# Optimization experiments

Measured on AMD Instinct MI355X. Metric: run time of the kernel, lower is better.

## Reference

```python
import jax, jax.numpy as jnp
import numpy as np

B, S, DIM, H, C = 1, 1024, 4096, 32, 8
HD = DIM // H  # 128
NEG = -1e9


def setup_inputs() -> dict:
    key = jax.random.key(0)
    ks = jax.random.split(key, 8)
    scale = 0.02
    x = jax.random.normal(ks[0], (B, S, DIM), jnp.float32)
    wq = jax.random.normal(ks[1], (DIM, DIM), jnp.float32) * scale
    wk = jax.random.normal(ks[2], (DIM, DIM), jnp.float32) * scale
    wv = jax.random.normal(ks[3], (DIM, DIM), jnp.float32) * scale
    wo = jax.random.normal(ks[4], (DIM, DIM), jnp.float32) * scale
    # RoPE tables (theta=10000), matching precompute_freqs_cis
    inv = 1.0 / (10000.0 ** (np.arange(0, HD, 2, dtype=np.float32) / HD))  # [HD/2]
    ang = np.arange(S, dtype=np.float32)[:, None] * inv[None, :]  # [S, HD/2]
    freqs_cos = jnp.asarray(np.cos(ang))
    freqs_sin = jnp.asarray(np.sin(ang))
    # causal mask used at prefill (start_pos == 0)
    mask = jnp.where(jnp.triu(jnp.ones((S, S), bool), k=1), jnp.float32(NEG), 0.0)
    # cluster labels: ensure every cluster non-empty; rep = first head with label
    rng = np.random.default_rng(0)
    lab = np.concatenate([np.arange(C), rng.integers(0, C, H - C)]).astype(np.int32)
    rep = np.array([np.where(lab == c)[0][0] for c in range(C)], dtype=np.int32)
    return {
        "x": x, "wq": wq, "wk": wk, "wv": wv, "wo": wo,
        "freqs_cos": freqs_cos, "freqs_sin": freqs_sin, "mask": mask,
        "cluster_assignment": jnp.asarray(lab), "rep_heads": jnp.asarray(rep),
        "start_pos": 0,
    }


def _rope(x, cos, sin):
    # x: [b, s, h, d]; cos/sin: [s, d/2]; interleaved complex multiply
    xr, xi = x[..., ::2], x[..., 1::2]
    cos = cos[None, :, None, :]
    sin = sin[None, :, None, :]
    orr = xr * cos - xi * sin
    oi = xr * sin + xi * cos
    return jnp.stack([orr, oi], axis=-1).reshape(x.shape)


def reference(x, wq, wk, wv, wo, freqs_cos, freqs_sin, mask,
              cluster_assignment, rep_heads, start_pos):
    b, s, dim = x.shape
    h, d = H, HD
    xq = (x @ wq.T).reshape(b, s, h, d)
    xk = (x @ wk.T).reshape(b, s, h, d)
    xv = (x @ wv.T).reshape(b, s, h, d)
    xq = _rope(xq, freqs_cos, freqs_sin)
    xk = _rope(xk, freqs_cos, freqs_sin)
    xqh = jnp.transpose(xq, (0, 2, 1, 3))  # [b, h, s, d]
    xkh = jnp.transpose(xk, (0, 2, 1, 3))
    vh = jnp.transpose(xv, (0, 2, 1, 3))
    # CHAI: gather representative head per cluster, score once per cluster
    xq_new = xqh[:, rep_heads]  # [b, C, s, d]
    xk_new = xkh[:, rep_heads]
    sc = jnp.einsum("bcqd,bckd->bcqk", xq_new, xk_new) / jnp.sqrt(jnp.float32(d))
    # scatter cluster scores back to every member head (pure gather by label)
    scores = sc[:, cluster_assignment]  # [b, h, s, s]
    scores = scores + mask[None, None]
    p = jax.nn.softmax(scores.astype(jnp.float32), axis=-1).astype(x.dtype)
    out = jnp.einsum("bhqk,bhkd->bhqd", p, vh)
    out = jnp.transpose(out, (0, 2, 1, 3)).reshape(b, s, h * d)
    return out @ wo.T
```

## Files before the change

kernel.cpp:

```cpp
#include <hip/hip_runtime.h>

typedef __bf16 bf16x8 __attribute__((ext_vector_type(8)));
typedef float f32x4 __attribute__((ext_vector_type(4)));

#define BM 128
#define BN 128
#define BK 64

__device__ __forceinline__ unsigned short f2bf(float f) {
    union { float f; unsigned int u; } x; x.f = f;
    unsigned int u = x.u;
    u += 0x7fffu + ((u >> 16) & 1u);
    return (unsigned short)(u >> 16);
}

__device__ __forceinline__ float bf2f(unsigned short h) {
    union { unsigned int u; float f; } x; x.u = ((unsigned int)h) << 16;
    return x.f;
}

__device__ __forceinline__ void async_copy16(const void* g, void* l) {
    __builtin_amdgcn_global_load_lds(
        (const __attribute__((address_space(1))) void*)(uintptr_t)g,
        (__attribute__((address_space(3))) void*)(uintptr_t)l, 16, 0, 0);
}

__global__ void cvt_all(const float* __restrict__ x, const float* __restrict__ wq,
                        const float* __restrict__ wk, const float* __restrict__ wv,
                        const float* __restrict__ wo, const int* __restrict__ rep,
                        unsigned short* __restrict__ xb, unsigned short* __restrict__ wqkvb,
                        unsigned short* __restrict__ wob) {
    long i = (long)blockIdx.x * 256 + threadIdx.x;
    const float* src;
    unsigned short* dst;
    long j;
    if (i < 1048576) {
        j = i;
        src = x; dst = xb;
    } else if (i < 7340032) {
        j = i - 1048576;
        int r = (int)(j >> 10), c4 = (int)(j & 1023);
        const float* s;
        if (r < 1024)      s = wq + ((long)(rep[r >> 7] * 128 + (r & 127)) << 12);
        else if (r < 2048) s = wk + ((long)(rep[(r - 1024) >> 7] * 128 + (r & 127)) << 12);
        else               s = wv + ((long)(r - 2048) << 12);
        float4 v = ((const float4*)s)[c4];
        ushort4 o = { f2bf(v.x), f2bf(v.y), f2bf(v.z), f2bf(v.w) };
        ((ushort4*)(wqkvb + ((long)r << 12)))[c4] = o;
        return;
    } else {
        j = i - 7340032;
        src = wo; dst = wob;
    }
    float4 v = ((const float4*)src)[j];
    ushort4 o = { f2bf(v.x), f2bf(v.y), f2bf(v.z), f2bf(v.w) };
    ((ushort4*)dst)[j] = o;
}


template<bool F32OUT, int MODE>
__global__ __launch_bounds__(256, 2) void gemm_bt(
    const unsigned short* __restrict__ A, const unsigned short* __restrict__ B,
    void* __restrict__ Cv, int K, int lda, int ldb, int ldc,
    long long aZ, long long bZ, long long cZ, const int* __restrict__ aIdx,
    int kOffZ, int nby) {
    __shared__ unsigned short As[BM * BK];
    __shared__ unsigned short Bs[BN * BK];

    int L = blockIdx.x;
    int q8 = gridDim.x >> 3;
    int wk_ = (L & 7) * q8 + (L >> 3);
    int bmi = wk_ & 7;
    int t2 = wk_ >> 3;
    int bni = t2 % nby;
    int z = t2 / nby;

    if (MODE == 1 && bni > bmi) return;

    A += (aIdx ? (long long)aIdx[z] : (long long)z) * aZ;
    B += (long long)z * bZ;
    int bm = bmi * BM;
    int bn = bni * BN;
    int t = threadIdx.x;
    int lane = t & 63;
    int w = t >> 6;
    int wr = (w >> 1) * 64, wc = (w & 1) * 64;

    int kt0 = z * kOffZ;
    int kEnd = kt0 + K;
    if (MODE == 2) kEnd = kt0 + min(K, bm + BM);

    f32x4 acc[4][4] = {};

    for (int kt = kt0; kt < kEnd; kt += BK) {
#pragma unroll
        for (int i = 0; i < 4; ++i) {
            int f = i * 256 + t;
            int row = f >> 3;
            int c8 = f & 7;
            async_copy16(A + (long)(bm + row) * lda + kt + c8 * 8, &As[f * 8]);
            async_copy16(B + (long)(bn + row) * ldb + kt + c8 * 8, &Bs[f * 8]);
        }
        asm volatile("s_waitcnt vmcnt(0)" ::: "memory");
        __syncthreads();
#pragma unroll
        for (int kk = 0; kk < BK; kk += 32) {
            bf16x8 a[4], b[4];
            int r0 = lane & 15;
            int kof = kk + ((lane >> 4) << 3);
#pragma unroll
            for (int m = 0; m < 4; ++m)
                a[m] = *(const bf16x8*)&As[(wr + m * 16 + r0) * BK + kof];
#pragma unroll
            for (int n = 0; n < 4; ++n)
                b[n] = *(const bf16x8*)&Bs[(wc + n * 16 + r0) * BK + kof];
#pragma unroll
            for (int m = 0; m < 4; ++m)
#pragma unroll
                for (int n = 0; n < 4; ++n)
                    acc[m][n] = __builtin_amdgcn_mfma_f32_16x16x32_bf16(a[m], b[n], acc[m][n], 0, 0, 0);
        }
        __syncthreads();
    }

    int cl = lane & 15;
    int rbase = (lane >> 4) << 2;
    if (F32OUT) {
        float* C = (float*)Cv + (long long)z * cZ;
#pragma unroll
        for (int m = 0; m < 4; ++m)
#pragma unroll
            for (int n = 0; n < 4; ++n)
#pragma unroll
                for (int j = 0; j < 4; ++j)
                    C[(long)(bm + wr + m * 16 + rbase + j) * ldc + (bn + wc + n * 16 + cl)] = acc[m][n][j];
    } else {
        unsigned short* C = (unsigned short*)Cv + (long long)z * cZ;
#pragma unroll
        for (int m = 0; m < 4; ++m)
#pragma unroll
            for (int n = 0; n < 4; ++n)
#pragma unroll
                for (int j = 0; j < 4; ++j)
                    C[(long)(bm + wr + m * 16 + rbase + j) * ldc + (bn + wc + n * 16 + cl)] = f2bf(acc[m][n][j]);
    }
}

__global__ void reduce_rope(unsigned short* __restrict__ qkv,
                            const float* __restrict__ fc, const float* __restrict__ fs,
                            int nsplit) {
    int s = blockIdx.y;
    int cc = (blockIdx.x * 256 + threadIdx.x) * 8;
    long base = (long)s * 6144 + cc;
    ushort4 a0 = *(const ushort4*)(qkv + base);
    ushort4 a1 = *(const ushort4*)(qkv + base + 4);
    float f[8] = { bf2f(a0.x), bf2f(a0.y), bf2f(a0.z), bf2f(a0.w),
                   bf2f(a1.x), bf2f(a1.y), bf2f(a1.z), bf2f(a1.w) };
    for (int z = 1; z < nsplit; ++z) {
        const unsigned short* p = qkv + (long)z * 6291456;
        ushort4 b0 = *(const ushort4*)(p + base);
        ushort4 b1 = *(const ushort4*)(p + base + 4);
        f[0] += bf2f(b0.x); f[1] += bf2f(b0.y); f[2] += bf2f(b0.z); f[3] += bf2f(b0.w);
        f[4] += bf2f(b1.x); f[5] += bf2f(b1.y); f[6] += bf2f(b1.z); f[7] += bf2f(b1.w);
    }
    if (cc < 2048) {
        int i0 = (cc & 127) >> 1;
        const float* cp = fc + (s << 6) + i0;
        const float* sp = fs + (s << 6) + i0;
#pragma unroll
        for (int p = 0; p < 4; ++p) {
            float co = cp[p], sn = sp[p];
            float x0 = f[2 * p], x1 = f[2 * p + 1];
            f[2 * p] = x0 * co - x1 * sn;
            f[2 * p + 1] = x0 * sn + x1 * co;
        }
    }
    ushort4 o0 = { f2bf(f[0]), f2bf(f[1]), f2bf(f[2]), f2bf(f[3]) };
    ushort4 o1 = { f2bf(f[4]), f2bf(f[5]), f2bf(f[6]), f2bf(f[7]) };
    *(ushort4*)(qkv + base) = o0;
    *(ushort4*)(qkv + base + 4) = o1;
}

__global__ void reduce_out4(const unsigned short* __restrict__ p, float* __restrict__ out) {
    long i = (long)blockIdx.x * 256 + threadIdx.x;
    ushort4 a = ((const ushort4*)p)[i];
    ushort4 b = ((const ushort4*)(p + 4194304))[i];
    ushort4 c = ((const ushort4*)(p + 8388608))[i];
    ushort4 d = ((const ushort4*)(p + 12582912))[i];
    float4 o;
    o.x = bf2f(a.x) + bf2f(b.x) + bf2f(c.x) + bf2f(d.x);
    o.y = bf2f(a.y) + bf2f(b.y) + bf2f(c.y) + bf2f(d.y);
    o.z = bf2f(a.z) + bf2f(b.z) + bf2f(c.z) + bf2f(d.z);
    o.w = bf2f(a.w) + bf2f(b.w) + bf2f(c.w) + bf2f(d.w);
    ((float4*)out)[i] = o;
}

__global__ void transpose_v(const unsigned short* __restrict__ qkv, unsigned short* __restrict__ vt) {
    __shared__ unsigned short tile[32][33];
    int h = blockIdx.z, d0 = blockIdx.x * 32, s0 = blockIdx.y * 32;
    int tx = threadIdx.x & 31, ty = threadIdx.x >> 5;
#pragma unroll
    for (int i = 0; i < 32; i += 8)
        tile[ty + i][tx] = qkv[(long)(s0 + ty + i) * 6144 + 2048 + h * 128 + d0 + tx];
    __syncthreads();
#pragma unroll
    for (int i = 0; i < 32; i += 8)
        vt[(long)h * 131072 + (long)(d0 + ty + i) * 1024 + s0 + tx] = tile[tx][ty + i];
}

__global__ __launch_bounds__(256) void softmax_causal(const float* __restrict__ sc,
                                                      unsigned short* __restrict__ P) {
    int i = blockIdx.x;
    int c = blockIdx.y;
    long base = ((long)c << 20) + ((long)i << 10);
    const float* row = sc + base;
    unsigned short* prow = P + base;
    int t = threadIdx.x;
    const float alpha = 0.08838834764831845f;
    int nj = i >> 8;

    float v[4];
    float mx = -3.4e38f;
    for (int j0 = 0; j0 <= nj; ++j0) {
        int j = j0 * 256 + t;
        float x = row[j] * alpha;
        v[j0] = (j <= i) ? x : -3.4e38f;
        mx = fmaxf(mx, v[j0]);
    }
#pragma unroll
    for (int o = 32; o > 0; o >>= 1) mx = fmaxf(mx, __shfl_xor(mx, o));
    __shared__ float red[4];
    int w = t >> 6, lane = t & 63;
    if (lane == 0) red[w] = mx;
    __syncthreads();
    mx = fmaxf(fmaxf(red[0], red[1]), fmaxf(red[2], red[3]));

    float e[4];
    float sum = 0.f;
    for (int j0 = 0; j0 <= nj; ++j0) {
        e[j0] = (v[j0] > -1e37f) ? __expf(v[j0] - mx) : 0.f;
        sum += e[j0];
    }
#pragma unroll
    for (int o = 32; o > 0; o >>= 1) sum += __shfl_xor(sum, o);
    __syncthreads();
    if (lane == 0) red[w] = sum;
    __syncthreads();
    sum = red[0] + red[1] + red[2] + red[3];
    float inv = 1.f / sum;
    for (int j0 = 0; j0 <= nj; ++j0) {
        int j = j0 * 256 + t;
        prow[j] = f2bf(e[j0] * inv);
    }
}


extern "C" void kernel_launch(void* const* d_in, const int* in_sizes, int n_in,
                              void* d_out, int out_size, void* d_ws, size_t ws_size,
                              hipStream_t stream) {
    const float* x  = (const float*)d_in[0];
    const float* wq = (const float*)d_in[1];
    const float* wk = (const float*)d_in[2];
    const float* wv = (const float*)d_in[3];
    const float* wo = (const float*)d_in[4];
    const float* fc = (const float*)d_in[5];
    const float* fs = (const float*)d_in[6];
    const int* lab = (const int*)d_in[8];
    const int* rep = (const int*)d_in[9];
    float* out = (float*)d_out;

    char* ws = (char*)d_ws;
    unsigned short* xb    = (unsigned short*)(ws);
    unsigned short* wqkvb = (unsigned short*)(ws + 8388608);
    unsigned short* wob   = (unsigned short*)(ws + 58720256);
    unsigned short* qkv_s = (unsigned short*)(ws + 92274688);
    unsigned short* vt    = (unsigned short*)(ws + 104857600);
    float* scores         = (float*)(ws + 8388608);
    unsigned short* P     = (unsigned short*)(ws + 41943040);
    unsigned short* opart = (unsigned short*)(ws + 8388608);
    unsigned short* attn  = xb;

    int skQ = (ws_size >= (size_t)142606336) ? 4
            : (ws_size >= (size_t)117440512) ? 2 : 1;

    cvt_all<<<45056, 256, 0, stream>>>(x, wq, wk, wv, wo, rep, xb, wqkvb, wob);

    if (skQ == 4) {
        gemm_bt<false, 0><<<1536, 256, 0, stream>>>(
            xb, wqkvb, qkv_s, 1024, 4096, 4096, 6144, 0, 0, 6291456, nullptr, 1024, 48);
    } else if (skQ == 2) {
        gemm_bt<false, 0><<<768, 256, 0, stream>>>(
            xb, wqkvb, qkv_s, 2048, 4096, 4096, 6144, 0, 0, 6291456, nullptr, 2048, 48);
    } else {
        gemm_bt<false, 0><<<384, 256, 0, stream>>>(
            xb, wqkvb, qkv_s, 4096, 4096, 4096, 6144, 0, 0, 0, nullptr, 0, 48);
    }

    reduce_rope<<<dim3(3, 1024), 256, 0, stream>>>(qkv_s, fc, fs, skQ);
    transpose_v<<<dim3(4, 32, 32), 256, 0, stream>>>(qkv_s, vt);

    gemm_bt<true, 1><<<512, 256, 0, stream>>>(
        qkv_s, qkv_s + 1024, scores, 128, 6144, 6144, 1024,
        128, 128, 1048576, nullptr, 0, 8);

    softmax_causal<<<dim3(1024, 8), 256, 0, stream>>>(scores, P);

    gemm_bt<false, 2><<<256, 256, 0, stream>>>(
        P, vt, attn, 1024, 1024, 1024, 4096,
        1048576, 131072, 128, lab, 0, 1);

    gemm_bt<false, 0><<<1024, 256, 0, stream>>>(
        attn, wob, opart, 1024, 4096, 4096, 4096, 0, 0, 4194304, nullptr, 1024, 32);
    reduce_out4<<<4096, 256, 0, stream>>>(opart, out);
}
```

Baseline: 225.5 us.

## Widen conversion vectors, store scores in bf16, cap QKV split-K at two

The fp32-to-bf16 conversion kernel now handles 8 elements per thread with 16-byte stores, halving the grid. The attention score GEMM writes bf16 instead of fp32, and softmax reads bf16, which halves score traffic at some cost in precision before the softmax. The QKV projection no longer uses 4-way split-K and uses at most 2-way, cutting partial-sum traffic but reducing parallelism.

```diff
diff --git a/kernel.cpp b/kernel.cpp
--- a/kernel.cpp
+++ b/kernel.cpp
@@ -2,6 +2,7 @@
 
 typedef __bf16 bf16x8 __attribute__((ext_vector_type(8)));
 typedef float f32x4 __attribute__((ext_vector_type(4)));
+typedef unsigned short u16x8 __attribute__((ext_vector_type(8)));
 
 #define BM 128
 #define BN 128
@@ -33,28 +34,28 @@
     long i = (long)blockIdx.x * 256 + threadIdx.x;
     const float* src;
     unsigned short* dst;
-    long j;
-    if (i < 1048576) {
-        j = i;
-        src = x; dst = xb;
-    } else if (i < 7340032) {
-        j = i - 1048576;
-        int r = (int)(j >> 10), c4 = (int)(j & 1023);
+    if (i < 524288) {
+        src = x + i * 8;
+        dst = xb + i * 8;
+    } else if (i < 3670016) {
+        long j = i - 524288;
+        int r = (int)(j >> 9), c8 = (int)(j & 511);
         const float* s;
         if (r < 1024)      s = wq + ((long)(rep[r >> 7] * 128 + (r & 127)) << 12);
         else if (r < 2048) s = wk + ((long)(rep[(r - 1024) >> 7] * 128 + (r & 127)) << 12);
         else               s = wv + ((long)(r - 2048) << 12);
-        float4 v = ((const float4*)s)[c4];
-        ushort4 o = { f2bf(v.x), f2bf(v.y), f2bf(v.z), f2bf(v.w) };
-        ((ushort4*)(wqkvb + ((long)r << 12)))[c4] = o;
-        return;
+        src = s + c8 * 8;
+        dst = wqkvb + ((long)r << 12) + c8 * 8;
     } else {
-        j = i - 7340032;
-        src = wo; dst = wob;
-    }
-    float4 v = ((const float4*)src)[j];
-    ushort4 o = { f2bf(v.x), f2bf(v.y), f2bf(v.z), f2bf(v.w) };
-    ((ushort4*)dst)[j] = o;
+        long j = i - 3670016;
+        src = wo + j * 8;
+        dst = wob + j * 8;
+    }
+    float4 v0 = ((const float4*)src)[0];
+    float4 v1 = ((const float4*)src)[1];
+    u16x8 o = { f2bf(v0.x), f2bf(v0.y), f2bf(v0.z), f2bf(v0.w),
+                f2bf(v1.x), f2bf(v1.y), f2bf(v1.z), f2bf(v1.w) };
+    *(u16x8*)dst = o;
 }
 
 
@@ -208,12 +209,12 @@
         vt[(long)h * 131072 + (long)(d0 + ty + i) * 1024 + s0 + tx] = tile[tx][ty + i];
 }
 
-__global__ __launch_bounds__(256) void softmax_causal(const float* __restrict__ sc,
+__global__ __launch_bounds__(256) void softmax_causal(const unsigned short* __restrict__ sc,
                                                       unsigned short* __restrict__ P) {
     int i = blockIdx.x;
     int c = blockIdx.y;
     long base = ((long)c << 20) + ((long)i << 10);
-    const float* row = sc + base;
+    const unsigned short* row = sc + base;
     unsigned short* prow = P + base;
     int t = threadIdx.x;
     const float alpha = 0.08838834764831845f;
@@ -223,7 +224,7 @@
     float mx = -3.4e38f;
     for (int j0 = 0; j0 <= nj; ++j0) {
         int j = j0 * 256 + t;
-        float x = row[j] * alpha;
+        float x = bf2f(row[j]) * alpha;
         v[j0] = (j <= i) ? x : -3.4e38f;
         mx = fmaxf(mx, v[j0]);
     }
@@ -275,20 +276,16 @@
     unsigned short* wob   = (unsigned short*)(ws + 58720256);
     unsigned short* qkv_s = (unsigned short*)(ws + 92274688);
     unsigned short* vt    = (unsigned short*)(ws + 104857600);
-    float* scores         = (float*)(ws + 8388608);
+    unsigned short* scores= (unsigned short*)(ws + 8388608);
     unsigned short* P     = (unsigned short*)(ws + 41943040);
     unsigned short* opart = (unsigned short*)(ws + 8388608);
     unsigned short* attn  = xb;
 
-    int skQ = (ws_size >= (size_t)142606336) ? 4
-            : (ws_size >= (size_t)117440512) ? 2 : 1;
-
-    cvt_all<<<45056, 256, 0, stream>>>(x, wq, wk, wv, wo, rep, xb, wqkvb, wob);
-
-    if (skQ == 4) {
-        gemm_bt<false, 0><<<1536, 256, 0, stream>>>(
-            xb, wqkvb, qkv_s, 1024, 4096, 4096, 6144, 0, 0, 6291456, nullptr, 1024, 48);
-    } else if (skQ == 2) {
+    int skQ = (ws_size >= (size_t)117440512) ? 2 : 1;
+
+    cvt_all<<<22528, 256, 0, stream>>>(x, wq, wk, wv, wo, rep, xb, wqkvb, wob);
+
+    if (skQ == 2) {
         gemm_bt<false, 0><<<768, 256, 0, stream>>>(
             xb, wqkvb, qkv_s, 2048, 4096, 4096, 6144, 0, 0, 6291456, nullptr, 2048, 48);
     } else {
@@ -299,7 +296,7 @@
     reduce_rope<<<dim3(3, 1024), 256, 0, stream>>>(qkv_s, fc, fs, skQ);
     transpose_v<<<dim3(4, 32, 32), 256, 0, stream>>>(qkv_s, vt);
 
-    gemm_bt<true, 1><<<512, 256, 0, stream>>>(
+    gemm_bt<false, 1><<<512, 256, 0, stream>>>(
         qkv_s, qkv_s + 1024, scores, 128, 6144, 6144, 1024,
         128, 128, 1048576, nullptr, 0, 8);
 
```

New measurement: 218.2 us. 1.03x faster.
